# Optimization experiments

Measured on AMD Instinct MI355X. Metric: run time of the kernel, lower is better.

Reference implementation:

```python
import jax, jax.numpy as jnp
import numpy as np

NQ = 100000  # Query nodes
NP = 100000  # Product nodes
E = 600000   # edges per relation
D_IN = 128
D_H = 128
# relation r: (src_type, dst_type); 0=Query, 1=Product
# 0: Click Q->P, 1: reverse_Click P->Q, 2: reverse_QueryResult P->Q, 3: QueryResult Q->P
REL = [(0, 1), (1, 0), (1, 0), (0, 1)]
N_NODES = [NQ, NP]


def setup_inputs() -> dict:
    key = jax.random.key(0)
    ks = jax.random.split(key, 12)
    s = 1.0 / np.sqrt(D_IN)  # keep activations well-scaled across 2 layers
    return {
        "x_query": jax.random.normal(ks[0], (NQ, D_IN), jnp.float32),
        "x_product": jax.random.normal(ks[1], (NP, D_IN), jnp.float32),
        "src_idx": jax.random.randint(ks[2], (4, E), 0, NQ, jnp.int32),
        "dst_idx": jax.random.randint(ks[3], (4, E), 0, NP, jnp.int32),
        "W_self1": jax.random.normal(ks[4], (4, D_IN, D_H), jnp.float32) * s,
        "W_neigh1": jax.random.normal(ks[5], (4, D_IN, D_H), jnp.float32) * s,
        "b1": jnp.zeros((4, D_H), jnp.float32),
        "W_self2": jax.random.normal(ks[6], (4, D_H, D_H), jnp.float32) * s,
        "W_neigh2": jax.random.normal(ks[7], (4, D_H, D_H), jnp.float32) * s,
        "b2": jnp.zeros((4, D_H), jnp.float32),
    }


def _hetero_sage_layer(h, W_self, W_neigh, b, src_idx, dst_idx):
    # h: [h_query, h_product]; per-relation SAGEConv(mean), cross-relation sum
    acc = [None, None]
    for r, (s, t) in enumerate(REL):
        nt = N_NODES[t]
        msg = h[s][src_idx[r]]                                   # [E, d] gather
        neigh_sum = jax.ops.segment_sum(msg, dst_idx[r], num_segments=nt)
        deg = jax.ops.segment_sum(jnp.ones((E,), h[s].dtype), dst_idx[r],
                                  num_segments=nt)
        neigh_mean = neigh_sum / jnp.maximum(deg, 1.0)[:, None]
        out = h[t] @ W_self[r] + neigh_mean @ W_neigh[r] + b[r]
        acc[t] = out if acc[t] is None else acc[t] + out
    return acc


def reference(x_query, x_product, src_idx, dst_idx,
              W_self1, W_neigh1, b1, W_self2, W_neigh2, b2):
    h = [x_query, x_product]
    h = _hetero_sage_layer(h, W_self1, W_neigh1, b1, src_idx, dst_idx)
    h = [jax.nn.relu(v) for v in h]  # ReLU only between layers
    h = _hetero_sage_layer(h, W_self2, W_neigh2, b2, src_idx, dst_idx)
    return (h[0], h[1])  # (H_query, H_product)
```

## Files before the change

### kernel.cpp

```cpp
#include <hip/hip_runtime.h>
#include <hip/hip_bf16.h>

#define N_NODES 100000
#define NEDGE   600000
#define SCAN_B  1024
#define NBLK    98
#define BSHIFT  9
#define NBUCK   196
#define BCAP    3456

typedef __attribute__((ext_vector_type(8))) short bf16x8;
typedef __attribute__((ext_vector_type(4))) short s16x4;
typedef __attribute__((ext_vector_type(4))) float f32x4;
typedef __attribute__((ext_vector_type(4))) unsigned u32x4;

__device__ __forceinline__ short f2bf(float f) {
  union { float f; unsigned u; } x; x.f = f;
  unsigned r = x.u + 0x7FFFu + ((x.u >> 16) & 1u);
  return (short)(r >> 16);
}

__global__ __launch_bounds__(256) void bin_k(const int* __restrict__ sidx,
                                             const int* __restrict__ didx,
                                             int* __restrict__ bincnt,
                                             unsigned* __restrict__ stage) {
  __shared__ int hist[NBUCK];
  __shared__ int base[NBUCK];
  int r = blockIdx.y, t = threadIdx.x;
  int e0 = blockIdx.x * 2048 + t;
  const int* dd = didx + (size_t)r * NEDGE;
  const int* ss = sidx + (size_t)r * NEDGE;
  for (int i = t; i < NBUCK; i += 256) hist[i] = 0;
  __syncthreads();
  unsigned pv[8]; int bu[8], lr[8];
#pragma unroll
  for (int j = 0; j < 8; ++j) {
    int e = e0 + j * 256;
    if (e < NEDGE) {
      int dv = dd[e];
      bu[j] = dv >> BSHIFT;
      pv[j] = (unsigned)ss[e] | ((unsigned)(dv & 511) << 17);
      lr[j] = atomicAdd(&hist[bu[j]], 1);
    }
  }
  __syncthreads();
  for (int i = t; i < NBUCK; i += 256)
    base[i] = atomicAdd(&bincnt[r * NBUCK + i], hist[i]);
  __syncthreads();
#pragma unroll
  for (int j = 0; j < 8; ++j) {
    int e = e0 + j * 256;
    if (e < NEDGE)
      stage[(size_t)(r * NBUCK + bu[j]) * BCAP + base[bu[j]] + lr[j]] = pv[j];
  }
}

__global__ __launch_bounds__(256) void hist_k(const unsigned* __restrict__ stage,
                                              const int* __restrict__ bincnt,
                                              int* __restrict__ cnt) {
  __shared__ int h[512];
  int bu = blockIdx.x, r = blockIdx.y, t = threadIdx.x;
  int len = bincnt[r * NBUCK + bu];
  const unsigned* sg = stage + (size_t)(r * NBUCK + bu) * BCAP;
  h[t] = 0; h[t + 256] = 0;
  __syncthreads();
  for (int i = t; i < len; i += 256) atomicAdd(&h[sg[i] >> 17], 1);
  __syncthreads();
  int lo = bu << BSHIFT;
  int d0 = lo + t;
  if (d0 < N_NODES)       cnt[r * N_NODES + d0]       = h[t];
  if (d0 + 256 < N_NODES) cnt[r * N_NODES + d0 + 256] = h[t + 256];
}

__global__ __launch_bounds__(256) void scan1_k(const int* __restrict__ cnt,
                                               int* __restrict__ bsum) {
  __shared__ int lds[256];
  int b = blockIdx.x, r = blockIdx.y, t = threadIdx.x;
  int i0 = b * SCAN_B + t * 4;
  int s = 0;
#pragma unroll
  for (int j = 0; j < 4; ++j)
    if (i0 + j < N_NODES) s += cnt[r * N_NODES + i0 + j];
  lds[t] = s;
  __syncthreads();
  for (int st = 128; st > 0; st >>= 1) {
    if (t < st) lds[t] += lds[t + st];
    __syncthreads();
  }
  if (t == 0) bsum[r * NBLK + b] = lds[0];
}

__global__ __launch_bounds__(128) void scan2_k(int* __restrict__ bsum) {
  __shared__ int buf[128];
  int t = threadIdx.x;
  for (int r = 0; r < 4; ++r) {
    int v = (t < NBLK) ? bsum[r * NBLK + t] : 0;
    buf[t] = v;
    __syncthreads();
    for (int st = 1; st < 128; st <<= 1) {
      int x = (t >= st) ? buf[t - st] : 0;
      __syncthreads();
      buf[t] += x;
      __syncthreads();
    }
    if (t < NBLK) bsum[r * NBLK + t] = buf[t] - v;
    __syncthreads();
  }
}

__global__ __launch_bounds__(256) void scan3_k(const int* __restrict__ cnt,
                                               const int* __restrict__ bsum,
                                               int* __restrict__ off) {
  __shared__ int lds[256];
  int b = blockIdx.x, r = blockIdx.y, t = threadIdx.x;
  int i0 = b * SCAN_B + t * 4;
  int c[4] = {0, 0, 0, 0};
#pragma unroll
  for (int j = 0; j < 4; ++j)
    if (i0 + j < N_NODES) c[j] = cnt[r * N_NODES + i0 + j];
  int s = c[0] + c[1] + c[2] + c[3];
  lds[t] = s;
  __syncthreads();
  for (int st = 1; st < 256; st <<= 1) {
    int x = (t >= st) ? lds[t - st] : 0;
    __syncthreads();
    lds[t] += x;
    __syncthreads();
  }
  int run = bsum[r * NBLK + b] + lds[t] - s;
  int* o = off + r * (N_NODES + 1);
#pragma unroll
  for (int j = 0; j < 4; ++j) {
    if (i0 + j < N_NODES) { o[i0 + j] = run; run += c[j]; }
  }
  if (b == 0 && t == 0) o[N_NODES] = NEDGE;
}

__global__ __launch_bounds__(256) void place_k(const unsigned* __restrict__ stage,
                                               const int* __restrict__ bincnt,
                                               const int* __restrict__ off,
                                               int* __restrict__ csr) {
  __shared__ int ofl[512];
  __shared__ int cur[512];
  int bu = blockIdx.x, r = blockIdx.y, t = threadIdx.x;
  int len = bincnt[r * NBUCK + bu];
  const unsigned* sg = stage + (size_t)(r * NBUCK + bu) * BCAP;
  const int* of = off + r * (N_NODES + 1);
  int* cs = csr + (size_t)r * NEDGE;
  int lo = bu << BSHIFT;
  int d0 = lo + t;
  ofl[t]       = (d0 < N_NODES) ? of[d0] : 0;
  ofl[t + 256] = (d0 + 256 < N_NODES) ? of[d0 + 256] : 0;
  cur[t] = 0; cur[t + 256] = 0;
  __syncthreads();
  for (int i = t; i < len; i += 256) {
    unsigned v = sg[i];
    int dl = v >> 17;
    int pos = ofl[dl] + atomicAdd(&cur[dl], 1);
    cs[pos] = (int)(v & 0x1FFFFu);
  }
}

__global__ __launch_bounds__(256) void cvt2_k(const float* __restrict__ x0,
                                              const float* __restrict__ x1,
                                              unsigned* __restrict__ o0,
                                              unsigned* __restrict__ o1) {
  const float* x = blockIdx.y ? x1 : x0;
  unsigned* o = blockIdx.y ? o1 : o0;
  int i = blockIdx.x * 256 + threadIdx.x;
  if (i >= N_NODES * 16) return;
  f32x4 v0 = ((const f32x4*)x)[i * 2];
  f32x4 v1 = ((const f32x4*)x)[i * 2 + 1];
  unsigned r0 = (unsigned)(unsigned short)f2bf(v0[0]) |
                ((unsigned)(unsigned short)f2bf(v0[1]) << 16);
  unsigned r1 = (unsigned)(unsigned short)f2bf(v0[2]) |
                ((unsigned)(unsigned short)f2bf(v0[3]) << 16);
  unsigned r2 = (unsigned)(unsigned short)f2bf(v1[0]) |
                ((unsigned)(unsigned short)f2bf(v1[1]) << 16);
  unsigned r3 = (unsigned)(unsigned short)f2bf(v1[2]) |
                ((unsigned)(unsigned short)f2bf(v1[3]) << 16);
  ((u32x4*)o)[i] = (u32x4){r0, r1, r2, r3};
}

__global__ __launch_bounds__(256) void prep_w_k(const float* __restrict__ Ws1,
                                                const float* __restrict__ Wn1,
                                                const float* __restrict__ Ws2,
                                                const float* __restrict__ Wn2,
                                                short* __restrict__ WTp) {
  int tid = blockIdx.x * 256 + threadIdx.x;
  int lane = tid & 63;
  int n0 = (tid >> 6) & 7;
  int idx3 = tid >> 9;
  int k0 = idx3 % 12;
  int lt = idx3 / 12;
  int l = lt >> 1, t = lt & 1;
  const float* Wself  = l ? Ws2 : Ws1;
  const float* Wneigh = l ? Wn2 : Wn1;
  int rA = t ? 0 : 1, rB = t ? 3 : 2;
  int n = n0 * 16 + (lane & 15);
  int kbase = k0 * 32 + (lane >> 4) * 8;
  short out[8];
#pragma unroll
  for (int j = 0; j < 8; ++j) {
    int k = kbase + j;
    int kk = k & 127, blk = k >> 7;
    float v;
    if (blk == 0)      v = Wself[rA * 16384 + kk * 128 + n] + Wself[rB * 16384 + kk * 128 + n];
    else if (blk == 1) v = Wneigh[rA * 16384 + kk * 128 + n];
    else               v = Wneigh[rB * 16384 + kk * 128 + n];
    out[j] = f2bf(v);
  }
  s16x4* dst = (s16x4*)&WTp[tid * 8];
  dst[0] = *(s16x4*)&out[0];
  dst[1] = *(s16x4*)&out[4];
}

__global__ __launch_bounds__(256) void prep_b_k(const float* __restrict__ b1,
                                                const float* __restrict__ b2,
                                                float* __restrict__ biasc) {
  int tid = blockIdx.x * 256 + threadIdx.x;
  if (tid >= 512) return;
  int l = tid >> 8, t = (tid >> 7) & 1, c = tid & 127;
  const float* b = l ? b2 : b1;
  int rA = t ? 0 : 1, rB = t ? 3 : 2;
  biasc[tid] = b[rA * 128 + c] + b[rB * 128 + c];
}

#define ACC8(u, a)                                            \
  {                                                           \
    _Pragma("unroll") for (int q = 0; q < 4; ++q) {           \
      union { unsigned w; float f; } lo_, hi_;                \
      lo_.w = (u)[q] << 16; hi_.w = (u)[q] & 0xffff0000u;     \
      (a)[2 * q] += lo_.f; (a)[2 * q + 1] += hi_.f;           \
    }                                                         \
  }

__device__ __forceinline__ int clampi(int q, int p0, int p1) {
  int t = q < p1 ? q : p0;
  return t < NEDGE ? t : 0;
}

__global__ __launch_bounds__(256) void gather2_k(
    const unsigned* __restrict__ src0, const unsigned* __restrict__ src1,
    const int* __restrict__ csr, const int* __restrict__ off,
    unsigned* __restrict__ m00, unsigned* __restrict__ m01,
    unsigned* __restrict__ m10, unsigned* __restrict__ m11) {
  int wv = __builtin_amdgcn_readfirstlane(threadIdx.x >> 6);
  int wid = blockIdx.x * 4 + wv;
  int lane = threadIdx.x & 63;
  int type = wid >= N_NODES;
  int n = type ? wid - N_NODES : wid;
  const unsigned* src = type ? src1 : src0;
  const int* csrA = csr + (type ? 0 : 1) * NEDGE;
  const int* csrB = csr + (type ? 3 : 2) * NEDGE;
  const int* offA = off + (type ? 0 : 1) * (N_NODES + 1);
  const int* offB = off + (type ? 3 : 2) * (N_NODES + 1);
  unsigned* mA = type ? m10 : m00;
  unsigned* mB = type ? m11 : m01;
  int pA0 = offA[n], pA1 = offA[n + 1];
  int pB0 = offB[n], pB1 = offB[n + 1];
  int degA = pA1 - pA0, degB = pB1 - pB0;
  int rowg = lane >> 4;
  int colg = lane & 15;
  float a[8] = {}, b[8] = {};
  {
    int ia0 = csrA[clampi(pA0 + rowg,     pA0, pA1)];
    int ia1 = csrA[clampi(pA0 + 4 + rowg, pA0, pA1)];
    int ib0 = csrB[clampi(pB0 + rowg,     pB0, pB1)];
    int ib1 = csrB[clampi(pB0 + 4 + rowg, pB0, pB1)];
    u32x4 ua0 = *(const u32x4*)(src + (size_t)ia0 * 64 + colg * 4);
    u32x4 ua1 = *(const u32x4*)(src + (size_t)ia1 * 64 + colg * 4);
    u32x4 ub0 = *(const u32x4*)(src + (size_t)ib0 * 64 + colg * 4);
    u32x4 ub1 = *(const u32x4*)(src + (size_t)ib1 * 64 + colg * 4);
    if (pA0 + rowg     < pA1) ACC8(ua0, a);
    if (pA0 + 4 + rowg < pA1) ACC8(ua1, a);
    if (pB0 + rowg     < pB1) ACC8(ub0, b);
    if (pB0 + 4 + rowg < pB1) ACC8(ub1, b);
  }
  for (int p = pA0 + 8; p < pA1; p += 8) {
    int i0 = csrA[clampi(p + rowg,     pA0, pA1)];
    int i1 = csrA[clampi(p + 4 + rowg, pA0, pA1)];
    u32x4 u0 = *(const u32x4*)(src + (size_t)i0 * 64 + colg * 4);
    u32x4 u1 = *(const u32x4*)(src + (size_t)i1 * 64 + colg * 4);
    if (p + rowg     < pA1) ACC8(u0, a);
    if (p + 4 + rowg < pA1) ACC8(u1, a);
  }
  for (int p = pB0 + 8; p < pB1; p += 8) {
    int i0 = csrB[clampi(p + rowg,     pB0, pB1)];
    int i1 = csrB[clampi(p + 4 + rowg, pB0, pB1)];
    u32x4 u0 = *(const u32x4*)(src + (size_t)i0 * 64 + colg * 4);
    u32x4 u1 = *(const u32x4*)(src + (size_t)i1 * 64 + colg * 4);
    if (p + rowg     < pB1) ACC8(u0, b);
    if (p + 4 + rowg < pB1) ACC8(u1, b);
  }
#pragma unroll
  for (int q = 0; q < 8; ++q) {
    a[q] += __shfl_xor(a[q], 16); a[q] += __shfl_xor(a[q], 32);
    b[q] += __shfl_xor(b[q], 16); b[q] += __shfl_xor(b[q], 32);
  }
  if (rowg == 0) {
    float invA = 1.0f / (float)(degA > 1 ? degA : 1);
    float invB = 1.0f / (float)(degB > 1 ? degB : 1);
    u32x4 wa, wb;
#pragma unroll
    for (int q = 0; q < 4; ++q) {
      wa[q] = (unsigned)(unsigned short)f2bf(a[2 * q] * invA) |
              ((unsigned)(unsigned short)f2bf(a[2 * q + 1] * invA) << 16);
      wb[q] = (unsigned)(unsigned short)f2bf(b[2 * q] * invB) |
              ((unsigned)(unsigned short)f2bf(b[2 * q + 1] * invB) << 16);
    }
    *(u32x4*)(mA + (size_t)n * 64 + colg * 4) = wa;
    *(u32x4*)(mB + (size_t)n * 64 + colg * 4) = wb;
  }
}

template<int OUT_RELU_BF16>
__global__ __launch_bounds__(256) void gemm2_k(
    const short* __restrict__ self0, const short* __restrict__ self1,
    const short* __restrict__ mA0, const short* __restrict__ mB0,
    const short* __restrict__ mA1, const short* __restrict__ mB1,
    const short* __restrict__ WTpL, const float* __restrict__ biascL,
    void* __restrict__ out0, void* __restrict__ out1) {
  __shared__ short Wlds[4 * 8 * 512];
  int type = blockIdx.y;
  const short* selfp = type ? self1 : self0;
  const short* meanA = type ? mA1 : mA0;
  const short* meanB = type ? mB1 : mB0;
  const short* WTp = WTpL + type * 49152;
  const float* biasc = biascL + type * 128;
  void* outp = type ? out1 : out0;
  int tid = threadIdx.x;
  int lane = tid & 63, wave = tid >> 6;
  int rowbase = blockIdx.x * 128 + wave * 32;
  int r0 = rowbase + (lane & 15), r1 = r0 + 16;
  int rc0 = r0 < N_NODES ? r0 : N_NODES - 1;
  int rc1 = r1 < N_NODES ? r1 : N_NODES - 1;
  int kg = lane >> 4;
  f32x4 acc[2][8] = {};
  for (int ch = 0; ch < 3; ++ch) {
    __syncthreads();
    const f32x4* s = (const f32x4*)WTp + ch * 2048;
    f32x4* dst = (f32x4*)Wlds;
#pragma unroll
    for (int i = 0; i < 8; ++i) dst[tid + i * 256] = s[tid + i * 256];
    __syncthreads();
    const short* mp = (ch == 0) ? selfp : ((ch == 1) ? meanA : meanB);
#pragma unroll
    for (int kh = 0; kh < 4; ++kh) {
      int kin = kh * 32 + kg * 8;
      bf16x8 a0 = *(const bf16x8*)(mp + (size_t)rc0 * 128 + kin);
      bf16x8 a1 = *(const bf16x8*)(mp + (size_t)rc1 * 128 + kin);
      const short* wb = &Wlds[kh * 4096 + lane * 8];
#pragma unroll
      for (int n0 = 0; n0 < 8; ++n0) {
        bf16x8 b = *(const bf16x8*)(wb + n0 * 512);
        acc[0][n0] = __builtin_amdgcn_mfma_f32_16x16x32_bf16(a0, b, acc[0][n0], 0, 0, 0);
        acc[1][n0] = __builtin_amdgcn_mfma_f32_16x16x32_bf16(a1, b, acc[1][n0], 0, 0, 0);
      }
    }
  }
  int colb = lane & 15, rloc = kg * 4;
#pragma unroll
  for (int mt = 0; mt < 2; ++mt) {
    int rb = rowbase + mt * 16 + rloc;
#pragma unroll
    for (int n0 = 0; n0 < 8; ++n0) {
      int cc = n0 * 16 + colb;
      float bv = biasc[cc];
#pragma unroll
      for (int j = 0; j < 4; ++j) {
        int rr = rb + j;
        if (rr < N_NODES) {
          float v = acc[mt][n0][j] + bv;
          if (OUT_RELU_BF16) {
            ((short*)outp)[(size_t)rr * 128 + cc] = f2bf(v > 0.f ? v : 0.f);
          } else {
            __builtin_nontemporal_store(v, (float*)outp + (size_t)rr * 128 + cc);
          }
        }
      }
    }
  }
}

extern "C" void kernel_launch(void* const* d_in, const int* in_sizes, int n_in,
                              void* d_out, int out_size, void* d_ws, size_t ws_size,
                              hipStream_t stream) {
  (void)in_sizes; (void)n_in; (void)out_size; (void)ws_size;
  const float* xq  = (const float*)d_in[0];
  const float* xp  = (const float*)d_in[1];
  const int*   src = (const int*)d_in[2];
  const int*   dst = (const int*)d_in[3];
  const float* Ws1 = (const float*)d_in[4];
  const float* Wn1 = (const float*)d_in[5];
  const float* b1  = (const float*)d_in[6];
  const float* Ws2 = (const float*)d_in[7];
  const float* Wn2 = (const float*)d_in[8];
  const float* b2  = (const float*)d_in[9];

  char* w = (char*)d_ws;
  int*   cnt    = (int*)w;      w += (size_t)4 * N_NODES * 4;
  int*   bincnt = (int*)w;      w += 4096;
  int*   off    = (int*)w;      w += (size_t)4 * (N_NODES + 1) * 4;
  int*   csr    = (int*)w;      w += (size_t)4 * NEDGE * 4;
  short* meanA  = (short*)w;    w += (size_t)N_NODES * 128 * 2;
  short* meanB  = (short*)w;    w += (size_t)N_NODES * 128 * 2;
  short* h1q    = (short*)w;    w += (size_t)N_NODES * 128 * 2;
  short* h1p    = (short*)w;    w += (size_t)N_NODES * 128 * 2;
  short* xqb    = (short*)w;    w += (size_t)N_NODES * 128 * 2;
  short* xpb    = (short*)w;    w += (size_t)N_NODES * 128 * 2;
  short* WTp    = (short*)w;    w += (size_t)4 * 49152 * 2;
  float* biasc  = (float*)w;    w += 512 * 4;
  int*   bsum   = (int*)w;      w += 4 * 128 * 4;
  unsigned* stage = (unsigned*)meanA;
  unsigned* mL1C = (unsigned*)d_out;
  unsigned* mL1D = mL1C + (size_t)N_NODES * 64;
  unsigned* mL2C = (unsigned*)xqb;
  unsigned* mL2D = (unsigned*)xpb;

  dim3 b256(256);
  const int bgrid = (NEDGE + 2047) / 2048;
  const int ggrid = (N_NODES + 127) / 128;
  const int wgrid = 2 * N_NODES / 4;
  const int cgrid = (N_NODES * 16 + 255) / 256;

  hipMemsetAsync(bincnt, 0, 4096, stream);
  bin_k<<<dim3(bgrid, 4), b256, 0, stream>>>(src, dst, bincnt, stage);
  hist_k<<<dim3(NBUCK, 4), b256, 0, stream>>>(stage, bincnt, cnt);
  scan1_k<<<dim3(NBLK, 4), b256, 0, stream>>>(cnt, bsum);
  scan2_k<<<dim3(1), dim3(128), 0, stream>>>(bsum);
  scan3_k<<<dim3(NBLK, 4), b256, 0, stream>>>(cnt, bsum, off);
  place_k<<<dim3(NBUCK, 4), b256, 0, stream>>>(stage, bincnt, off, csr);
  prep_w_k<<<dim3(384), b256, 0, stream>>>(Ws1, Wn1, Ws2, Wn2, WTp);
  prep_b_k<<<dim3(2), b256, 0, stream>>>(b1, b2, biasc);
  cvt2_k<<<dim3(cgrid, 2), b256, 0, stream>>>(xq, xp, (unsigned*)xqb, (unsigned*)xpb);

  gather2_k<<<wgrid, b256, 0, stream>>>((const unsigned*)xpb, (const unsigned*)xqb,
      csr, off, (unsigned*)meanA, (unsigned*)meanB, mL1C, mL1D);
  gemm2_k<1><<<dim3(ggrid, 2), b256, 0, stream>>>(
      xqb, xpb, meanA, meanB, (const short*)mL1C, (const short*)mL1D,
      WTp, biasc, h1q, h1p);

  gather2_k<<<wgrid, b256, 0, stream>>>((const unsigned*)h1p, (const unsigned*)h1q,
      csr, off, (unsigned*)meanA, (unsigned*)meanB, mL2C, mL2D);
  gemm2_k<0><<<dim3(ggrid, 2), b256, 0, stream>>>(
      h1q, h1p, meanA, meanB, (const short*)mL2C, (const short*)mL2D,
      WTp + 2 * 49152, biasc + 256,
      (float*)d_out, (float*)d_out + (size_t)N_NODES * 128);
}
```

Before: 471.3 us.

## Pad CSR neighbor lists to multiples of eight with a zero sentinel row

Each node's neighbor list in the CSR is padded to a multiple of 8 (minimum 8), and the padding slots point to an all-zero extra row appended to each feature buffer. The gather kernel can then drop per-element bounds clamping and predicated accumulation, and reads degree from the count array instead. The bf16 packing also switches to the hardware v_cvt_pk_bf16_f32 instruction. In exchange there is a larger CSR, an extra padfill kernel, extra memsets, and wasted loads of the zero row for low-degree nodes.

```diff
diff --git a/kernel.cpp b/kernel.cpp
--- a/kernel.cpp
+++ b/kernel.cpp
@@ -8,6 +8,8 @@
 #define BSHIFT  9
 #define NBUCK   196
 #define BCAP    3456
+#define PADCAP  1400000
+#define ZROW    N_NODES
 
 typedef __attribute__((ext_vector_type(8))) short bf16x8;
 typedef __attribute__((ext_vector_type(4))) short s16x4;
@@ -18,6 +20,12 @@
   union { float f; unsigned u; } x; x.f = f;
   unsigned r = x.u + 0x7FFFu + ((x.u >> 16) & 1u);
   return (short)(r >> 16);
+}
+
+__device__ __forceinline__ unsigned cvtpk(float lo, float hi) {
+  unsigned r;
+  asm("v_cvt_pk_bf16_f32 %0, %1, %2" : "=v"(r) : "v"(lo), "v"(hi));
+  return r;
 }
 
 __global__ __launch_bounds__(256) void bin_k(const int* __restrict__ sidx,
@@ -72,6 +80,11 @@
   if (d0 + 256 < N_NODES) cnt[r * N_NODES + d0 + 256] = h[t + 256];
 }
 
+__device__ __forceinline__ int padlen8(int c) {
+  int p = (c + 7) & ~7;
+  return p < 8 ? 8 : p;
+}
+
 __global__ __launch_bounds__(256) void scan1_k(const int* __restrict__ cnt,
                                                int* __restrict__ bsum) {
   __shared__ int lds[256];
@@ -80,7 +93,7 @@
   int s = 0;
 #pragma unroll
   for (int j = 0; j < 4; ++j)
-    if (i0 + j < N_NODES) s += cnt[r * N_NODES + i0 + j];
+    if (i0 + j < N_NODES) s += padlen8(cnt[r * N_NODES + i0 + j]);
   lds[t] = s;
   __syncthreads();
   for (int st = 128; st > 0; st >>= 1) {
@@ -110,14 +123,14 @@
 
 __global__ __launch_bounds__(256) void scan3_k(const int* __restrict__ cnt,
                                                const int* __restrict__ bsum,
-                                               int* __restrict__ off) {
+                                               int* __restrict__ offp) {
   __shared__ int lds[256];
   int b = blockIdx.x, r = blockIdx.y, t = threadIdx.x;
   int i0 = b * SCAN_B + t * 4;
   int c[4] = {0, 0, 0, 0};
 #pragma unroll
   for (int j = 0; j < 4; ++j)
-    if (i0 + j < N_NODES) c[j] = cnt[r * N_NODES + i0 + j];
+    if (i0 + j < N_NODES) c[j] = padlen8(cnt[r * N_NODES + i0 + j]);
   int s = c[0] + c[1] + c[2] + c[3];
   lds[t] = s;
   __syncthreads();
@@ -128,25 +141,28 @@
     __syncthreads();
   }
   int run = bsum[r * NBLK + b] + lds[t] - s;
-  int* o = off + r * (N_NODES + 1);
+  int* o = offp + r * (N_NODES + 1);
 #pragma unroll
   for (int j = 0; j < 4; ++j) {
-    if (i0 + j < N_NODES) { o[i0 + j] = run; run += c[j]; }
-  }
-  if (b == 0 && t == 0) o[N_NODES] = NEDGE;
+    int i = i0 + j;
+    if (i < N_NODES) {
+      o[i] = run; run += c[j];
+      if (i == N_NODES - 1) o[N_NODES] = run;
+    }
+  }
 }
 
 __global__ __launch_bounds__(256) void place_k(const unsigned* __restrict__ stage,
                                                const int* __restrict__ bincnt,
-                                               const int* __restrict__ off,
-                                               int* __restrict__ csr) {
+                                               const int* __restrict__ offp,
+                                               int* __restrict__ csrp) {
   __shared__ int ofl[512];
   __shared__ int cur[512];
   int bu = blockIdx.x, r = blockIdx.y, t = threadIdx.x;
   int len = bincnt[r * NBUCK + bu];
   const unsigned* sg = stage + (size_t)(r * NBUCK + bu) * BCAP;
-  const int* of = off + r * (N_NODES + 1);
-  int* cs = csr + (size_t)r * NEDGE;
+  const int* of = offp + r * (N_NODES + 1);
+  int* cs = csrp + (size_t)r * PADCAP;
   int lo = bu << BSHIFT;
   int d0 = lo + t;
   ofl[t]       = (d0 < N_NODES) ? of[d0] : 0;
@@ -159,6 +175,19 @@
     int pos = ofl[dl] + atomicAdd(&cur[dl], 1);
     cs[pos] = (int)(v & 0x1FFFFu);
   }
+}
+
+__global__ __launch_bounds__(256) void padfill_k(const int* __restrict__ cnt,
+                                                 const int* __restrict__ offp,
+                                                 int* __restrict__ csrp) {
+  int n = blockIdx.x * 256 + threadIdx.x;
+  int r = blockIdx.y;
+  if (n >= N_NODES) return;
+  int d = cnt[r * N_NODES + n];
+  const int* o = offp + r * (N_NODES + 1);
+  int p = o[n] + d, p1 = o[n + 1];
+  int* cs = csrp + (size_t)r * PADCAP;
+  for (; p < p1; ++p) cs[p] = ZROW;
 }
 
 __global__ __launch_bounds__(256) void cvt2_k(const float* __restrict__ x0,
@@ -171,15 +200,8 @@
   if (i >= N_NODES * 16) return;
   f32x4 v0 = ((const f32x4*)x)[i * 2];
   f32x4 v1 = ((const f32x4*)x)[i * 2 + 1];
-  unsigned r0 = (unsigned)(unsigned short)f2bf(v0[0]) |
-                ((unsigned)(unsigned short)f2bf(v0[1]) << 16);
-  unsigned r1 = (unsigned)(unsigned short)f2bf(v0[2]) |
-                ((unsigned)(unsigned short)f2bf(v0[3]) << 16);
-  unsigned r2 = (unsigned)(unsigned short)f2bf(v1[0]) |
-                ((unsigned)(unsigned short)f2bf(v1[1]) << 16);
-  unsigned r3 = (unsigned)(unsigned short)f2bf(v1[2]) |
-                ((unsigned)(unsigned short)f2bf(v1[3]) << 16);
-  ((u32x4*)o)[i] = (u32x4){r0, r1, r2, r3};
+  ((u32x4*)o)[i] = (u32x4){cvtpk(v0[0], v0[1]), cvtpk(v0[2], v0[3]),
+                           cvtpk(v1[0], v1[1]), cvtpk(v1[2], v1[3])};
 }
 
 __global__ __launch_bounds__(256) void prep_w_k(const float* __restrict__ Ws1,
@@ -235,14 +257,10 @@
     }                                                         \
   }
 
-__device__ __forceinline__ int clampi(int q, int p0, int p1) {
-  int t = q < p1 ? q : p0;
-  return t < NEDGE ? t : 0;
-}
-
 __global__ __launch_bounds__(256) void gather2_k(
     const unsigned* __restrict__ src0, const unsigned* __restrict__ src1,
-    const int* __restrict__ csr, const int* __restrict__ off,
+    const int* __restrict__ csrp, const int* __restrict__ offp,
+    const int* __restrict__ cnt,
     unsigned* __restrict__ m00, unsigned* __restrict__ m01,
     unsigned* __restrict__ m10, unsigned* __restrict__ m11) {
   int wv = __builtin_amdgcn_readfirstlane(threadIdx.x >> 6);
@@ -251,47 +269,40 @@
   int type = wid >= N_NODES;
   int n = type ? wid - N_NODES : wid;
   const unsigned* src = type ? src1 : src0;
-  const int* csrA = csr + (type ? 0 : 1) * NEDGE;
-  const int* csrB = csr + (type ? 3 : 2) * NEDGE;
-  const int* offA = off + (type ? 0 : 1) * (N_NODES + 1);
-  const int* offB = off + (type ? 3 : 2) * (N_NODES + 1);
+  int rA = type ? 0 : 1, rB = type ? 3 : 2;
+  const int* csrA = csrp + (size_t)rA * PADCAP;
+  const int* csrB = csrp + (size_t)rB * PADCAP;
+  const int* offA = offp + rA * (N_NODES + 1);
+  const int* offB = offp + rB * (N_NODES + 1);
+  int degA = cnt[rA * N_NODES + n];
+  int degB = cnt[rB * N_NODES + n];
   unsigned* mA = type ? m10 : m00;
   unsigned* mB = type ? m11 : m01;
   int pA0 = offA[n], pA1 = offA[n + 1];
   int pB0 = offB[n], pB1 = offB[n + 1];
-  int degA = pA1 - pA0, degB = pB1 - pB0;
   int rowg = lane >> 4;
   int colg = lane & 15;
   float a[8] = {}, b[8] = {};
   {
-    int ia0 = csrA[clampi(pA0 + rowg,     pA0, pA1)];
-    int ia1 = csrA[clampi(pA0 + 4 + rowg, pA0, pA1)];
-    int ib0 = csrB[clampi(pB0 + rowg,     pB0, pB1)];
-    int ib1 = csrB[clampi(pB0 + 4 + rowg, pB0, pB1)];
+    int ia0 = csrA[pA0 + rowg], ia1 = csrA[pA0 + 4 + rowg];
+    int ib0 = csrB[pB0 + rowg], ib1 = csrB[pB0 + 4 + rowg];
     u32x4 ua0 = *(const u32x4*)(src + (size_t)ia0 * 64 + colg * 4);
     u32x4 ua1 = *(const u32x4*)(src + (size_t)ia1 * 64 + colg * 4);
     u32x4 ub0 = *(const u32x4*)(src + (size_t)ib0 * 64 + colg * 4);
     u32x4 ub1 = *(const u32x4*)(src + (size_t)ib1 * 64 + colg * 4);
-    if (pA0 + rowg     < pA1) ACC8(ua0, a);
-    if (pA0 + 4 + rowg < pA1) ACC8(ua1, a);
-    if (pB0 + rowg     < pB1) ACC8(ub0, b);
-    if (pB0 + 4 + rowg < pB1) ACC8(ub1, b);
+    ACC8(ua0, a); ACC8(ua1, a); ACC8(ub0, b); ACC8(ub1, b);
   }
   for (int p = pA0 + 8; p < pA1; p += 8) {
-    int i0 = csrA[clampi(p + rowg,     pA0, pA1)];
-    int i1 = csrA[clampi(p + 4 + rowg, pA0, pA1)];
+    int i0 = csrA[p + rowg], i1 = csrA[p + 4 + rowg];
     u32x4 u0 = *(const u32x4*)(src + (size_t)i0 * 64 + colg * 4);
     u32x4 u1 = *(const u32x4*)(src + (size_t)i1 * 64 + colg * 4);
-    if (p + rowg     < pA1) ACC8(u0, a);
-    if (p + 4 + rowg < pA1) ACC8(u1, a);
+    ACC8(u0, a); ACC8(u1, a);
   }
   for (int p = pB0 + 8; p < pB1; p += 8) {
-    int i0 = csrB[clampi(p + rowg,     pB0, pB1)];
-    int i1 = csrB[clampi(p + 4 + rowg, pB0, pB1)];
+    int i0 = csrB[p + rowg], i1 = csrB[p + 4 + rowg];
     u32x4 u0 = *(const u32x4*)(src + (size_t)i0 * 64 + colg * 4);
     u32x4 u1 = *(const u32x4*)(src + (size_t)i1 * 64 + colg * 4);
-    if (p + rowg     < pB1) ACC8(u0, b);
-    if (p + 4 + rowg < pB1) ACC8(u1, b);
+    ACC8(u0, b); ACC8(u1, b);
   }
 #pragma unroll
   for (int q = 0; q < 8; ++q) {
@@ -304,10 +315,8 @@
     u32x4 wa, wb;
 #pragma unroll
     for (int q = 0; q < 4; ++q) {
-      wa[q] = (unsigned)(unsigned short)f2bf(a[2 * q] * invA) |
-              ((unsigned)(unsigned short)f2bf(a[2 * q + 1] * invA) << 16);
-      wb[q] = (unsigned)(unsigned short)f2bf(b[2 * q] * invB) |
-              ((unsigned)(unsigned short)f2bf(b[2 * q + 1] * invB) << 16);
+      wa[q] = cvtpk(a[2 * q] * invA, a[2 * q + 1] * invA);
+      wb[q] = cvtpk(b[2 * q] * invB, b[2 * q + 1] * invB);
     }
     *(u32x4*)(mA + (size_t)n * 64 + colg * 4) = wa;
     *(u32x4*)(mB + (size_t)n * 64 + colg * 4) = wb;
@@ -401,14 +410,14 @@
   char* w = (char*)d_ws;
   int*   cnt    = (int*)w;      w += (size_t)4 * N_NODES * 4;
   int*   bincnt = (int*)w;      w += 4096;
-  int*   off    = (int*)w;      w += (size_t)4 * (N_NODES + 1) * 4;
-  int*   csr    = (int*)w;      w += (size_t)4 * NEDGE * 4;
+  int*   offp   = (int*)w;      w += (size_t)4 * (N_NODES + 1) * 4;
+  int*   csrp   = (int*)w;      w += (size_t)4 * PADCAP * 4;
   short* meanA  = (short*)w;    w += (size_t)N_NODES * 128 * 2;
   short* meanB  = (short*)w;    w += (size_t)N_NODES * 128 * 2;
-  short* h1q    = (short*)w;    w += (size_t)N_NODES * 128 * 2;
-  short* h1p    = (short*)w;    w += (size_t)N_NODES * 128 * 2;
-  short* xqb    = (short*)w;    w += (size_t)N_NODES * 128 * 2;
-  short* xpb    = (short*)w;    w += (size_t)N_NODES * 128 * 2;
+  short* h1q    = (short*)w;    w += (size_t)(N_NODES + 1) * 128 * 2;
+  short* h1p    = (short*)w;    w += (size_t)(N_NODES + 1) * 128 * 2;
+  short* xqb    = (short*)w;    w += (size_t)(N_NODES + 1) * 128 * 2;
+  short* xpb    = (short*)w;    w += (size_t)(N_NODES + 1) * 128 * 2;
   short* WTp    = (short*)w;    w += (size_t)4 * 49152 * 2;
   float* biasc  = (float*)w;    w += 512 * 4;
   int*   bsum   = (int*)w;      w += 4 * 128 * 4;
@@ -423,26 +432,32 @@
   const int ggrid = (N_NODES + 127) / 128;
   const int wgrid = 2 * N_NODES / 4;
   const int cgrid = (N_NODES * 16 + 255) / 256;
+  const int ngrid = (N_NODES + 255) / 256;
 
   hipMemsetAsync(bincnt, 0, 4096, stream);
+  hipMemsetAsync(xqb + (size_t)N_NODES * 128, 0, 256, stream);
+  hipMemsetAsync(xpb + (size_t)N_NODES * 128, 0, 256, stream);
+  hipMemsetAsync(h1q + (size_t)N_NODES * 128, 0, 256, stream);
+  hipMemsetAsync(h1p + (size_t)N_NODES * 128, 0, 256, stream);
   bin_k<<<dim3(bgrid, 4), b256, 0, stream>>>(src, dst, bincnt, stage);
   hist_k<<<dim3(NBUCK, 4), b256, 0, stream>>>(stage, bincnt, cnt);
   scan1_k<<<dim3(NBLK, 4), b256, 0, stream>>>(cnt, bsum);
   scan2_k<<<dim3(1), dim3(128), 0, stream>>>(bsum);
-  scan3_k<<<dim3(NBLK, 4), b256, 0, stream>>>(cnt, bsum, off);
-  place_k<<<dim3(NBUCK, 4), b256, 0, stream>>>(stage, bincnt, off, csr);
+  scan3_k<<<dim3(NBLK, 4), b256, 0, stream>>>(cnt, bsum, offp);
+  place_k<<<dim3(NBUCK, 4), b256, 0, stream>>>(stage, bincnt, offp, csrp);
+  padfill_k<<<dim3(ngrid, 4), b256, 0, stream>>>(cnt, offp, csrp);
   prep_w_k<<<dim3(384), b256, 0, stream>>>(Ws1, Wn1, Ws2, Wn2, WTp);
   prep_b_k<<<dim3(2), b256, 0, stream>>>(b1, b2, biasc);
   cvt2_k<<<dim3(cgrid, 2), b256, 0, stream>>>(xq, xp, (unsigned*)xqb, (unsigned*)xpb);
 
   gather2_k<<<wgrid, b256, 0, stream>>>((const unsigned*)xpb, (const unsigned*)xqb,
-      csr, off, (unsigned*)meanA, (unsigned*)meanB, mL1C, mL1D);
+      csrp, offp, cnt, (unsigned*)meanA, (unsigned*)meanB, mL1C, mL1D);
   gemm2_k<1><<<dim3(ggrid, 2), b256, 0, stream>>>(
       xqb, xpb, meanA, meanB, (const short*)mL1C, (const short*)mL1D,
       WTp, biasc, h1q, h1p);
 
   gather2_k<<<wgrid, b256, 0, stream>>>((const unsigned*)h1p, (const unsigned*)h1q,
-      csr, off, (unsigned*)meanA, (unsigned*)meanB, mL2C, mL2D);
+      csrp, offp, cnt, (unsigned*)meanA, (unsigned*)meanB, mL2C, mL2D);
   gemm2_k<0><<<dim3(ggrid, 2), b256, 0, stream>>>(
       h1q, h1p, meanA, meanB, (const short*)mL2C, (const short*)mL2D,
       WTp + 2 * 49152, biasc + 256,
```

Result: slower. 487.9 us (+3.5%).

## Double-buffer weight tiles in LDS for GEMM and use packed bf16 convert

Applied to the files above, without the earlier changes.

The GEMM kernel now splits its weight staging into six half-size chunks held in two LDS buffers. The next chunk is prefetched into registers while MFMAs run on the current one, which is meant to overlap global weight loads with compute and halve the LDS footprint. Separately, manual float-to-bf16 rounding is replaced by the hardware v_cvt_pk_bf16_f32 instruction in the convert and aggregation kernels. The cost is more barriers and extra register staging, and the hardware convert's rounding may differ subtly from the manual round-to-nearest-even.

```diff
diff --git a/kernel.cpp b/kernel.cpp
--- a/kernel.cpp
+++ b/kernel.cpp
@@ -18,6 +18,12 @@
   union { float f; unsigned u; } x; x.f = f;
   unsigned r = x.u + 0x7FFFu + ((x.u >> 16) & 1u);
   return (short)(r >> 16);
+}
+
+__device__ __forceinline__ unsigned cvtpk(float lo, float hi) {
+  unsigned r;
+  asm("v_cvt_pk_bf16_f32 %0, %1, %2" : "=v"(r) : "v"(lo), "v"(hi));
+  return r;
 }
 
 __global__ __launch_bounds__(256) void bin_k(const int* __restrict__ sidx,
@@ -171,15 +177,8 @@
   if (i >= N_NODES * 16) return;
   f32x4 v0 = ((const f32x4*)x)[i * 2];
   f32x4 v1 = ((const f32x4*)x)[i * 2 + 1];
-  unsigned r0 = (unsigned)(unsigned short)f2bf(v0[0]) |
-                ((unsigned)(unsigned short)f2bf(v0[1]) << 16);
-  unsigned r1 = (unsigned)(unsigned short)f2bf(v0[2]) |
-                ((unsigned)(unsigned short)f2bf(v0[3]) << 16);
-  unsigned r2 = (unsigned)(unsigned short)f2bf(v1[0]) |
-                ((unsigned)(unsigned short)f2bf(v1[1]) << 16);
-  unsigned r3 = (unsigned)(unsigned short)f2bf(v1[2]) |
-                ((unsigned)(unsigned short)f2bf(v1[3]) << 16);
-  ((u32x4*)o)[i] = (u32x4){r0, r1, r2, r3};
+  ((u32x4*)o)[i] = (u32x4){cvtpk(v0[0], v0[1]), cvtpk(v0[2], v0[3]),
+                           cvtpk(v1[0], v1[1]), cvtpk(v1[2], v1[3])};
 }
 
 __global__ __launch_bounds__(256) void prep_w_k(const float* __restrict__ Ws1,
@@ -304,10 +303,8 @@
     u32x4 wa, wb;
 #pragma unroll
     for (int q = 0; q < 4; ++q) {
-      wa[q] = (unsigned)(unsigned short)f2bf(a[2 * q] * invA) |
-              ((unsigned)(unsigned short)f2bf(a[2 * q + 1] * invA) << 16);
-      wb[q] = (unsigned)(unsigned short)f2bf(b[2 * q] * invB) |
-              ((unsigned)(unsigned short)f2bf(b[2 * q + 1] * invB) << 16);
+      wa[q] = cvtpk(a[2 * q] * invA, a[2 * q + 1] * invA);
+      wb[q] = cvtpk(b[2 * q] * invB, b[2 * q + 1] * invB);
     }
     *(u32x4*)(mA + (size_t)n * 64 + colg * 4) = wa;
     *(u32x4*)(mB + (size_t)n * 64 + colg * 4) = wb;
@@ -321,7 +318,7 @@
     const short* __restrict__ mA1, const short* __restrict__ mB1,
     const short* __restrict__ WTpL, const float* __restrict__ biascL,
     void* __restrict__ out0, void* __restrict__ out1) {
-  __shared__ short Wlds[4 * 8 * 512];
+  __shared__ short Wlds[2][8192];
   int type = blockIdx.y;
   const short* selfp = type ? self1 : self0;
   const short* meanA = type ? mA1 : mA0;
@@ -337,20 +334,30 @@
   int rc1 = r1 < N_NODES ? r1 : N_NODES - 1;
   int kg = lane >> 4;
   f32x4 acc[2][8] = {};
-  for (int ch = 0; ch < 3; ++ch) {
-    __syncthreads();
-    const f32x4* s = (const f32x4*)WTp + ch * 2048;
-    f32x4* dst = (f32x4*)Wlds;
-#pragma unroll
-    for (int i = 0; i < 8; ++i) dst[tid + i * 256] = s[tid + i * 256];
-    __syncthreads();
-    const short* mp = (ch == 0) ? selfp : ((ch == 1) ? meanA : meanB);
-#pragma unroll
-    for (int kh = 0; kh < 4; ++kh) {
-      int kin = kh * 32 + kg * 8;
+  const f32x4* Wsrc = (const f32x4*)WTp;
+  f32x4 st[4];
+#pragma unroll
+  for (int j = 0; j < 4; ++j) st[j] = Wsrc[tid + j * 256];
+  {
+    f32x4* d = (f32x4*)Wlds[0];
+#pragma unroll
+    for (int j = 0; j < 4; ++j) d[tid + j * 256] = st[j];
+  }
+  __syncthreads();
+  for (int c = 0; c < 6; ++c) {
+    if (c < 5) {
+#pragma unroll
+      for (int j = 0; j < 4; ++j) st[j] = Wsrc[(c + 1) * 1024 + tid + j * 256];
+    }
+    const short* mp = (c < 2) ? selfp : ((c < 4) ? meanA : meanB);
+    const short* wbase = Wlds[c & 1];
+#pragma unroll
+    for (int kh = 0; kh < 2; ++kh) {
+      int kk = (c * 2 + kh) & 3;
+      int kin = kk * 32 + kg * 8;
       bf16x8 a0 = *(const bf16x8*)(mp + (size_t)rc0 * 128 + kin);
       bf16x8 a1 = *(const bf16x8*)(mp + (size_t)rc1 * 128 + kin);
-      const short* wb = &Wlds[kh * 4096 + lane * 8];
+      const short* wb = wbase + kh * 4096 + lane * 8;
 #pragma unroll
       for (int n0 = 0; n0 < 8; ++n0) {
         bf16x8 b = *(const bf16x8*)(wb + n0 * 512);
@@ -358,6 +365,12 @@
         acc[1][n0] = __builtin_amdgcn_mfma_f32_16x16x32_bf16(a1, b, acc[1][n0], 0, 0, 0);
       }
     }
+    if (c < 5) {
+      f32x4* d = (f32x4*)Wlds[(c + 1) & 1];
+#pragma unroll
+      for (int j = 0; j < 4; ++j) d[tid + j * 256] = st[j];
+    }
+    __syncthreads();
   }
   int colb = lane & 15, rloc = kg * 4;
 #pragma unroll
```

New measurement: 469.0 us. About the same (-0.5%).
